# Performance work log

Measured on AMD Instinct MI355X. Metric: run time of the kernel, lower is better.

## Reference

```python
import math
import jax, jax.numpy as jnp
import numpy as np

IN_CH = 256
OUT_CH = 256
K = 7
DILATION = 8
PADDING = 28
STRIDE = 1
GROUPS = 1
L_DIL = K * DILATION  # effective dilated kernel length (56)


def setup_inputs() -> dict:
    key = jax.random.key(0)
    k1, k2, k3, k4 = jax.random.split(key, 4)
    x = jax.random.normal(k1, (32, IN_CH, 4096), dtype=jnp.float32)
    # kaiming_uniform_(a=sqrt(5)) on [O, C/g, K] -> bound = sqrt(6/((1+5)*fan_in)) = 1/sqrt(fan_in)
    fan_in = (IN_CH // GROUPS) * K
    wb = 1.0 / math.sqrt(fan_in)
    weight = jax.random.uniform(k2, (OUT_CH, IN_CH // GROUPS, K), jnp.float32, -wb, wb)
    bias = jax.random.uniform(k3, (OUT_CH,), jnp.float32, -wb, wb)
    # P init: -int(K*d/2) + i*d, plus sub-dilation jitter so subpixel interpolation is exercised
    base = -(L_DIL // 2) + jnp.arange(K, dtype=jnp.float32) * DILATION  # [K]
    jitter = jax.random.uniform(k4, (OUT_CH, IN_CH // GROUPS, K), jnp.float32, -0.45, 0.45) * DILATION
    P = jnp.broadcast_to(base, (OUT_CH, IN_CH // GROUPS, K)) + jitter
    return {"input": x, "weight": weight, "P": P, "bias": bias}


def _build_kernel(weight, P):
    # SurrogateDilation1d, subpixel interpolation, 'add' overlapping, 'clamp' border:
    # scatter each weight tap at continuous position P into a dense [O, C/g, L_DIL] kernel
    # with linear interpolation between floor(P) and floor(P)+1.
    pos = jnp.clip(P + (L_DIL // 2), 0.0, L_DIL - 1)       # [O, C, K], clamp border
    lo = jnp.floor(pos)
    frac = pos - lo                                        # grad flows to P (floor grad is 0)
    lo_i = lo.astype(jnp.int32)
    hi_i = jnp.minimum(lo_i + 1, L_DIL - 1)
    O, C, _ = weight.shape
    oi = jnp.arange(O)[:, None, None]
    ci = jnp.arange(C)[None, :, None]
    kernel = jnp.zeros((O, C, L_DIL), weight.dtype)
    kernel = kernel.at[oi, ci, lo_i].add(weight * (1.0 - frac))
    kernel = kernel.at[oi, ci, hi_i].add(weight * frac)
    return kernel


def reference(input, weight, P, bias):
    kernel = _build_kernel(weight, P)  # [O, C/g, L_DIL]
    out = jax.lax.conv_general_dilated(
        input, kernel,
        window_strides=(STRIDE,),
        padding=[(PADDING, PADDING)],
        dimension_numbers=("NCH", "OIH", "NCH"),
        feature_group_count=GROUPS,
    )
    return out + bias[None, :, None]
```

## Files before the change

### kernel.cpp

```cpp
#include <hip/hip_runtime.h>
#include <hip/hip_bf16.h>
#include <stdint.h>
#include <stddef.h>

#define LIN   4096
#define TOUT  4097
#define NBATCH 32
#define TPAD  4416
#define MT    128
#define NT    256
#define XROWS (NT + 56)
#define LMAX  53

typedef __attribute__((ext_vector_type(8)))  short short8;
typedef __attribute__((ext_vector_type(16))) float float16;

#define XT_ELEMS ((size_t)NBATCH * TPAD * 256)
#define XT_BYTES (XT_ELEMS * 2)

__global__ __launch_bounds__(256) void pad_kernel(__hip_bfloat16* __restrict__ xT) {
  const int b = blockIdx.x;
  const size_t r0 = blockIdx.y ? 4124 : 0;
  int4* p = (int4*)(xT + ((size_t)b * TPAD + r0) * 256);
  for (int f = threadIdx.x; f < 28 * 256 * 2 / 16; f += 256)
    p[f] = int4{0, 0, 0, 0};
}

__global__ __launch_bounds__(256) void xpose_kernel(const float* __restrict__ x,
                                                    __hip_bfloat16* __restrict__ xT) {
  const int t0  = blockIdx.x * 64;
  const int b   = blockIdx.y;
  const int tid = threadIdx.x;
  __shared__ __hip_bfloat16 tile[64 * 66];
  for (int c0 = 0; c0 < 256; c0 += 64) {
#pragma unroll
    for (int j = 0; j < 16; ++j) {
      int f = j * 256 + tid;
      int c_l = f >> 6, t_l = f & 63;
      float v = x[((size_t)(b * 256 + c0 + c_l)) * LIN + t0 + t_l];
      tile[t_l * 66 + c_l] = __float2bfloat16(v);
    }
    __syncthreads();
    const unsigned short* tp = (const unsigned short*)tile;
#pragma unroll
    for (int j = 0; j < 8; ++j) {
      int f = j * 256 + tid;
      int t_l = f >> 5, c2 = (f & 31) << 1;
      uint32_t v = (uint32_t)tp[t_l * 66 + c2] | ((uint32_t)tp[t_l * 66 + c2 + 1] << 16);
      *(uint32_t*)&xT[((size_t)(b * TPAD + 28 + t0 + t_l)) * 256 + c0 + c2] = v;
    }
    __syncthreads();
  }
}

__global__ __launch_bounds__(256) void build_kd(const float* __restrict__ w,
                                                const float* __restrict__ P,
                                                __hip_bfloat16* __restrict__ Kd) {
  const int o = blockIdx.x;
  const int c = threadIdx.x;
  __shared__ float accs[256 * 57];
  float* a = &accs[c * 57];
  for (int l = 0; l < 56; ++l) a[l] = 0.0f;
  const int base = (o * 256 + c) * 7;
#pragma unroll
  for (int k = 0; k < 7; ++k) {
    float wv  = w[base + k];
    float pos = P[base + k] + 28.0f;
    pos = fminf(fmaxf(pos, 0.0f), 55.0f);
    float lo  = floorf(pos);
    float fr  = pos - lo;
    int li = (int)lo;
    int hi = li + 1; if (hi > 55) hi = 55;
    a[li] += wv * (1.0f - fr);
    a[hi] += wv * fr;
  }
  const int cu = c >> 3, e = c & 7;
  for (int l = 0; l < 56; ++l) {
    size_t idx = (((size_t)(l * 32 + cu) * 256 + o) << 3) + e;
    Kd[idx] = __float2bfloat16(a[l]);
  }
}

__global__ __launch_bounds__(256, 2) void conv_mfma(const __hip_bfloat16* __restrict__ xT,
                                                    const __hip_bfloat16* __restrict__ Kd,
                                                    const float* __restrict__ bias,
                                                    float* __restrict__ out) {
  __shared__ __hip_bfloat16 xs[XROWS * 64];

  const int tid  = threadIdx.x;
  const int t0   = blockIdx.x * NT;
  const int b    = blockIdx.y;
  const int o0   = blockIdx.z * MT;
  const int wid  = tid >> 6;
  const int lane = tid & 63;
  const int m_off = (wid & 1) * 64;
  const int n_off = (wid >> 1) * 128;
  const int laneN = lane & 31;
  const int half  = lane >> 5;
  const int rbase = n_off + laneN;

  const uint32_t voff = (uint32_t)((half * 256 + m_off + laneN) << 4);

  float16 acc[2][4];
#pragma unroll
  for (int i = 0; i < 2; ++i)
#pragma unroll
    for (int j = 0; j < 4; ++j) acc[i][j] = (float16)(0.0f);

  short8 aR[2][2];
  short8 bR[2][4];

#define STEP_A(n0, n1, c0, c1, base)                                    \
  asm volatile("global_load_dwordx4 %0, %4, %5\n\t"                     \
               "global_load_dwordx4 %1, %4, %5 offset:512\n\t"          \
               "s_waitcnt vmcnt(2)"                                     \
               : "=&v"(n0), "=&v"(n1), "+v"(c0), "+v"(c1)               \
               : "v"(voff), "s"(base))
#define ISSUE_A(n0, n1, base)                                           \
  asm volatile("global_load_dwordx4 %0, %2, %3\n\t"                     \
               "global_load_dwordx4 %1, %2, %3 offset:512"              \
               : "=&v"(n0), "=&v"(n1)                                   \
               : "v"(voff), "s"(base))
#define DRAIN_A(c0, c1)                                                 \
  asm volatile("s_waitcnt vmcnt(0)" : "+v"(c0), "+v"(c1))

  for (int cc = 0; cc < 4; ++cc) {
    if (cc) __syncthreads();
    {
      const size_t gbase = ((size_t)(b * TPAD + t0)) * 256 + cc * 64;
#pragma unroll
      for (int j = 0; j < 10; ++j) {
        int f = j * 256 + tid;
        if (f < XROWS * 8) {
          int r = f >> 3, u = f & 7;
          int4 v = *(const int4*)(xT + gbase + (size_t)r * 256 + u * 8);
          *(int4*)((char*)xs + r * 128 + ((u ^ (r & 7)) << 4)) = v;
        }
      }
    }
    __syncthreads();
    auto loadB4 = [&](short8 (&dst)[4], int L, int kk) {
      const int rb = rbase + L;
      const char* p_ = (const char*)xs + rb * 128 +
                       ((((kk << 1) + half) ^ (rb & 7)) << 4);
#pragma unroll
      for (int jn = 0; jn < 4; ++jn)
        dst[jn] = *(const short8*)(p_ + jn * 4096);
    };

    uint64_t abase = (uint64_t)(uintptr_t)Kd + (uint32_t)(cc << 15) + (uint32_t)(o0 << 4);

    loadB4(bR[0], 0, 0);
    ISSUE_A(aR[0][0], aR[0][1], abase);
    abase += 8192;

    for (int l = 0; l < LMAX; ++l) {
#pragma unroll
      for (int kk = 0; kk < 4; ++kk) {
        const int cur = kk & 1, nxt = cur ^ 1;
        if (kk < 3) {
          loadB4(bR[nxt], l, kk + 1);
          STEP_A(aR[nxt][0], aR[nxt][1], aR[cur][0], aR[cur][1], abase);
          abase += (kk == 2) ? 106496 : 8192;
        } else if (l + 1 < LMAX) {
          loadB4(bR[nxt], l + 1, 0);
          STEP_A(aR[nxt][0], aR[nxt][1], aR[cur][0], aR[cur][1], abase);
          abase += 8192;
        } else {
          DRAIN_A(aR[cur][0], aR[cur][1]);
        }
        __builtin_amdgcn_sched_barrier(0);
        __builtin_amdgcn_s_setprio(1);
#pragma unroll
        for (int i = 0; i < 2; ++i)
#pragma unroll
          for (int jn = 0; jn < 4; ++jn)
            acc[i][jn] = __builtin_amdgcn_mfma_f32_32x32x16_bf16(aR[cur][i], bR[cur][jn], acc[i][jn], 0, 0, 0);
        __builtin_amdgcn_s_setprio(0);
      }
    }
  }
#undef STEP_A
#undef ISSUE_A
#undef DRAIN_A

#pragma unroll
  for (int i = 0; i < 2; ++i) {
#pragma unroll
    for (int jn = 0; jn < 4; ++jn) {
      int t = t0 + n_off + jn * 32 + laneN;
#pragma unroll
      for (int r = 0; r < 16; ++r) {
        int row = (r & 3) + 8 * (r >> 2) + 4 * half;
        int o = o0 + m_off + i * 32 + row;
        out[((size_t)(b * 256 + o)) * TOUT + t] = acc[i][jn][r] + bias[o];
      }
    }
  }
}

__global__ __launch_bounds__(256) void edge_kernel(const __hip_bfloat16* __restrict__ xT,
                                                   const float* __restrict__ w,
                                                   const float* __restrict__ P,
                                                   const float* __restrict__ bias,
                                                   float* __restrict__ out) {
  const int o = blockIdx.x;
  const int c = threadIdx.x;
  __shared__ float swlo[7 * 256], swhi[7 * 256];
  __shared__ int   sil[7 * 256],  sih[7 * 256];
  const int base = (o * 256 + c) * 7;
#pragma unroll
  for (int k = 0; k < 7; ++k) {
    float wv  = w[base + k];
    float pos = fminf(fmaxf(P[base + k] + 28.0f, 0.0f), 55.0f);
    float lo  = floorf(pos);
    float fr  = pos - lo;
    int li = (int)lo;
    int hi = li + 1; if (hi > 55) hi = 55;
    swlo[k * 256 + c] = wv * (1.0f - fr);
    swhi[k * 256 + c] = wv * fr;
    sil[k * 256 + c]  = li;
    sih[k * 256 + c]  = hi;
  }
  __syncthreads();
  const int wid = c >> 6, lane = c & 63;
#pragma unroll
  for (int bi = 0; bi < 8; ++bi) {
    const int b = wid * 8 + bi;
    const __hip_bfloat16* xrow = xT + ((size_t)b * TPAD + 4096) * 256;
    float acc = 0.0f;
#pragma unroll
    for (int cj = 0; cj < 4; ++cj) {
      const int cx = cj * 64 + lane;
#pragma unroll
      for (int k = 0; k < 7; ++k) {
        const int idx = k * 256 + cx;
        acc += swlo[idx] * __bfloat162float(xrow[(size_t)sil[idx] * 256 + cx])
             + swhi[idx] * __bfloat162float(xrow[(size_t)sih[idx] * 256 + cx]);
      }
    }
#pragma unroll
    for (int off = 32; off > 0; off >>= 1) acc += __shfl_down(acc, off, 64);
    if (lane == 0) out[((size_t)(b * 256 + o)) * TOUT + 4096] = acc + bias[o];
  }
}

extern "C" void kernel_launch(void* const* d_in, const int* in_sizes, int n_in,
                              void* d_out, int out_size, void* d_ws, size_t ws_size,
                              hipStream_t stream) {
  const float* x    = (const float*)d_in[0];
  const float* w    = (const float*)d_in[1];
  const float* P    = (const float*)d_in[2];
  const float* bias = (const float*)d_in[3];
  float* out = (float*)d_out;

  __hip_bfloat16* xT = (__hip_bfloat16*)d_ws;
  __hip_bfloat16* Kd = (__hip_bfloat16*)((char*)d_ws + XT_BYTES);

  pad_kernel<<<dim3(NBATCH, 2), 256, 0, stream>>>(xT);
  xpose_kernel<<<dim3(LIN / 64, NBATCH), 256, 0, stream>>>(x, xT);
  build_kd<<<dim3(256), 256, 0, stream>>>(w, P, Kd);
  conv_mfma<<<dim3(LIN / NT, NBATCH, 256 / MT), 256, 0, stream>>>(xT, Kd, bias, out);
  edge_kernel<<<dim3(256), 256, 0, stream>>>(xT, w, P, bias, out);
}
```

Before: 942.0 us.

## Deepen weight prefetch to two stages and use strip-major LDS layout

Changes the shared-memory tile of transposed input from a row-major XOR-swizzled layout to a strip-per-16-byte-column layout (stride 5040 bytes), so B operand addresses become simple pointer increments. Also deepens the global weight-operand prefetch from one stage to two (four register buffers, waitcnt vmcnt(4)) to hide more global-load latency behind MFMA work. This costs extra VGPRs for the additional A buffers, which may pressure occupancy at launch bounds of two blocks per SIMD group. The new LDS layout may also introduce bank conflicts.

After: 886.6 us. -5.9%, faster.

```diff
diff --git a/kernel.cpp b/kernel.cpp
--- a/kernel.cpp
+++ b/kernel.cpp
@@ -11,6 +11,7 @@
 #define NT    256
 #define XROWS (NT + 56)
 #define LMAX  53
+#define STRIP 5040
 
 typedef __attribute__((ext_vector_type(8)))  short short8;
 typedef __attribute__((ext_vector_type(16))) float float16;
@@ -85,7 +86,8 @@
                                                     const __hip_bfloat16* __restrict__ Kd,
                                                     const float* __restrict__ bias,
                                                     float* __restrict__ out) {
-  __shared__ __hip_bfloat16 xs[XROWS * 64];
+  __shared__ int4 xs2i[8 * STRIP / 16];
+  char* xs2 = (char*)xs2i;
 
   const int tid  = threadIdx.x;
   const int t0   = blockIdx.x * NT;
@@ -97,7 +99,6 @@
   const int n_off = (wid >> 1) * 128;
   const int laneN = lane & 31;
   const int half  = lane >> 5;
-  const int rbase = n_off + laneN;
 
   const uint32_t voff = (uint32_t)((half * 256 + m_off + laneN) << 4);
 
@@ -107,13 +108,13 @@
 #pragma unroll
     for (int j = 0; j < 4; ++j) acc[i][j] = (float16)(0.0f);
 
-  short8 aR[2][2];
+  short8 aR[4][2];
   short8 bR[2][4];
 
 #define STEP_A(n0, n1, c0, c1, base)                                    \
   asm volatile("global_load_dwordx4 %0, %4, %5\n\t"                     \
                "global_load_dwordx4 %1, %4, %5 offset:512\n\t"          \
-               "s_waitcnt vmcnt(2)"                                     \
+               "s_waitcnt vmcnt(4)"                                     \
                : "=&v"(n0), "=&v"(n1), "+v"(c0), "+v"(c1)               \
                : "v"(voff), "s"(base))
 #define ISSUE_A(n0, n1, base)                                           \
@@ -121,7 +122,9 @@
                "global_load_dwordx4 %1, %2, %3 offset:512"              \
                : "=&v"(n0), "=&v"(n1)                                   \
                : "v"(voff), "s"(base))
-#define DRAIN_A(c0, c1)                                                 \
+#define TAIL_A2(c0, c1)                                                 \
+  asm volatile("s_waitcnt vmcnt(2)" : "+v"(c0), "+v"(c1))
+#define TAIL_A0(c0, c1)                                                 \
   asm volatile("s_waitcnt vmcnt(0)" : "+v"(c0), "+v"(c1))
 
   for (int cc = 0; cc < 4; ++cc) {
@@ -134,40 +137,40 @@
         if (f < XROWS * 8) {
           int r = f >> 3, u = f & 7;
           int4 v = *(const int4*)(xT + gbase + (size_t)r * 256 + u * 8);
-          *(int4*)((char*)xs + r * 128 + ((u ^ (r & 7)) << 4)) = v;
+          *(int4*)(xs2 + u * STRIP + r * 16) = v;
         }
       }
     }
     __syncthreads();
-    auto loadB4 = [&](short8 (&dst)[4], int L, int kk) {
-      const int rb = rbase + L;
-      const char* p_ = (const char*)xs + rb * 128 +
-                       ((((kk << 1) + half) ^ (rb & 7)) << 4);
+
+    const char* pB = xs2 + (n_off + laneN) * 16 + half * STRIP;
+
+    auto loadB4 = [&](short8 (&dst)[4], const char* p_) {
 #pragma unroll
       for (int jn = 0; jn < 4; ++jn)
-        dst[jn] = *(const short8*)(p_ + jn * 4096);
+        dst[jn] = *(const short8*)(p_ + jn * 512);
     };
 
     uint64_t abase = (uint64_t)(uintptr_t)Kd + (uint32_t)(cc << 15) + (uint32_t)(o0 << 4);
 
-    loadB4(bR[0], 0, 0);
-    ISSUE_A(aR[0][0], aR[0][1], abase);
-    abase += 8192;
+    ISSUE_A(aR[0][0], aR[0][1], abase); abase += 8192;
+    ISSUE_A(aR[1][0], aR[1][1], abase); abase += 8192;
+    loadB4(bR[0], pB);
 
     for (int l = 0; l < LMAX; ++l) {
 #pragma unroll
       for (int kk = 0; kk < 4; ++kk) {
         const int cur = kk & 1, nxt = cur ^ 1;
-        if (kk < 3) {
-          loadB4(bR[nxt], l, kk + 1);
-          STEP_A(aR[nxt][0], aR[nxt][1], aR[cur][0], aR[cur][1], abase);
-          abase += (kk == 2) ? 106496 : 8192;
-        } else if (l + 1 < LMAX) {
-          loadB4(bR[nxt], l + 1, 0);
-          STEP_A(aR[nxt][0], aR[nxt][1], aR[cur][0], aR[cur][1], abase);
-          abase += 8192;
+        if (kk < 3)              loadB4(bR[nxt], pB + (kk + 1) * 10080);
+        else if (l + 1 < LMAX)   loadB4(bR[nxt], pB + 16);
+        if (kk < 2 || l + 1 < LMAX) {
+          STEP_A(aR[(kk + 2) & 3][0], aR[(kk + 2) & 3][1],
+                 aR[kk][0], aR[kk][1], abase);
+          abase += (kk == 1) ? 106496 : 8192;
+        } else if (kk == 2) {
+          TAIL_A2(aR[2][0], aR[2][1]);
         } else {
-          DRAIN_A(aR[cur][0], aR[cur][1]);
+          TAIL_A0(aR[3][0], aR[3][1]);
         }
         __builtin_amdgcn_sched_barrier(0);
         __builtin_amdgcn_s_setprio(1);
@@ -175,14 +178,16 @@
         for (int i = 0; i < 2; ++i)
 #pragma unroll
           for (int jn = 0; jn < 4; ++jn)
-            acc[i][jn] = __builtin_amdgcn_mfma_f32_32x32x16_bf16(aR[cur][i], bR[cur][jn], acc[i][jn], 0, 0, 0);
+            acc[i][jn] = __builtin_amdgcn_mfma_f32_32x32x16_bf16(aR[kk][i], bR[cur][jn], acc[i][jn], 0, 0, 0);
         __builtin_amdgcn_s_setprio(0);
       }
+      pB += 16;
     }
   }
 #undef STEP_A
 #undef ISSUE_A
-#undef DRAIN_A
+#undef TAIL_A2
+#undef TAIL_A0
 
 #pragma unroll
   for (int i = 0; i < 2; ++i) {
```
